# Performance work log

Measured on AMD Instinct MI355X. Metric: run time of the kernel, lower is better.

## Reference

```python
import jax, jax.numpy as jnp
import numpy as np

B, T, C, H = 2, 2048, 1024, 16
D = C // H  # head dim = 64
EPS = 1e-6  # kernel adds 1e-6 to softmax denominator


def setup_inputs() -> dict:
    key = jax.random.key(0)
    k1, k2, k3, k4, k5 = jax.random.split(key, 5)
    s = 1.0 / np.sqrt(C)
    return {
        "x": jax.random.normal(k1, (B, T, C), dtype=jnp.float32),
        "w_attn": jax.random.normal(k2, (3 * C, C), dtype=jnp.float32) * s,
        "b_attn": jax.random.normal(k3, (3 * C,), dtype=jnp.float32) * 0.02,
        "w_proj": jax.random.normal(k4, (C, C), dtype=jnp.float32) * s,
        "b_proj": jax.random.normal(k5, (C,), dtype=jnp.float32) * 0.02,
    }


def reference(x, w_attn, b_attn, w_proj, b_proj):
    b, t, c = x.shape
    qkv = x @ w_attn.T + b_attn                      # [B,T,3C]
    q, k, v = jnp.split(qkv, 3, axis=2)
    # [B,T,C] -> [B,H,T,D]
    q = q.reshape(b, t, H, D).transpose(0, 2, 1, 3)
    k = k.reshape(b, t, H, D).transpose(0, 2, 1, 3)
    v = v.reshape(b, t, H, D).transpose(0, 2, 1, 3)
    scale = 1.0 / np.sqrt(D)
    att = jnp.einsum("bhid,bhjd->bhij", q, k) * scale  # [B,H,T,T]
    causal = jnp.tril(jnp.ones((t, t), dtype=bool))
    att = jnp.where(causal, att, -jnp.inf)
    # softmax matching the HIP kernel: denom has +1e-6
    m = jnp.max(att, axis=-1, keepdims=True)
    e = jnp.exp(att - m)                             # masked entries -> 0
    p = e / (jnp.sum(e, axis=-1, keepdims=True) + EPS)
    y = jnp.einsum("bhij,bhjd->bhid", p, v)          # [B,H,T,D]
    y = y.transpose(0, 2, 1, 3).reshape(b, t, c)     # [B,T,C]
    return y @ w_proj.T + b_proj
```

## Files before the change

### kernel.cpp

```cpp
#include <hip/hip_runtime.h>

#define B_ 2
#define T_ 2048
#define C_ 1024
#define H_ 16
#define D_ 64

typedef __bf16 bf16x8 __attribute__((ext_vector_type(8)));
typedef float f32x4 __attribute__((ext_vector_type(4)));

__device__ __forceinline__ unsigned short f2bf(float f) {
  unsigned u = __float_as_uint(f);
  unsigned r = (u + 0x7fffu + ((u >> 16) & 1u)) >> 16;
  return (unsigned short)r;
}

#define NX 1048576
#define NWA 786432
#define NWP 262144
__global__ __launch_bounds__(256) void convert_all(
    const float* __restrict__ x, const float* __restrict__ wa,
    const float* __restrict__ wp, unsigned short* __restrict__ xb,
    unsigned short* __restrict__ wab, unsigned short* __restrict__ wpb) {
  int i = blockIdx.x * 256 + threadIdx.x;
  const float* s; unsigned short* d; int j;
  if (i < NX)            { s = x;  d = xb;  j = i; }
  else if (i < NX + NWA) { s = wa; d = wab; j = i - NX; }
  else                   { s = wp; d = wpb; j = i - NX - NWA; }
  float4 v = ((const float4*)s)[j];
  ushort4 u;
  u.x = f2bf(v.x); u.y = f2bf(v.y); u.z = f2bf(v.z); u.w = f2bf(v.w);
  ((ushort4*)d)[j] = u;
}

__global__ __launch_bounds__(256) void gemm_bt(
    const unsigned short* __restrict__ A,
    const unsigned short* __restrict__ Bm,
    const float* __restrict__ bias,
    int M, int N, int K, int mode,
    float* __restrict__ outf,
    unsigned short* __restrict__ qb,
    unsigned short* __restrict__ kb,
    unsigned short* __restrict__ vb) {
  __shared__ unsigned short As[128 * 64];
  __shared__ unsigned short Bs[128 * 64];

  const int tid  = threadIdx.x;
  const int lane = tid & 63;
  const int wave = tid >> 6;
  const int quad = lane >> 4;
  const int l16  = lane & 15;
  const int q4   = quad * 4;

  const int bm = blockIdx.y * 128;
  const int bn = blockIdx.x * 128;
  const int wm = (wave >> 1) * 64;
  const int wn = (wave & 1) * 64;

  f32x4 acc[4][4] = {};

  const int srow8 = lane >> 3;
  const int scol  = ((lane & 7) ^ srow8) * 8;
  const int srow  = wave * 8 + srow8;

  for (int k0 = 0; k0 < K; k0 += 64) {
#pragma unroll
    for (int c = 0; c < 4; ++c) {
      const int r = c * 32 + srow;
      const unsigned short* ga = A  + (size_t)(bm + r) * K + (k0 + scol);
      const unsigned short* gb = Bm + (size_t)(bn + r) * K + (k0 + scol);
      unsigned short* la = &As[(c * 32 + wave * 8) * 64];
      unsigned short* lb = &Bs[(c * 32 + wave * 8) * 64];
      __builtin_amdgcn_global_load_lds(
          (__attribute__((address_space(1))) unsigned int*)ga,
          (__attribute__((address_space(3))) unsigned int*)la, 16, 0, 0);
      __builtin_amdgcn_global_load_lds(
          (__attribute__((address_space(1))) unsigned int*)gb,
          (__attribute__((address_space(3))) unsigned int*)lb, 16, 0, 0);
    }
    __syncthreads();
#pragma unroll
    for (int ks = 0; ks < 2; ++ks) {
      bf16x8 af[4], bfr[4];
#pragma unroll
      for (int i = 0; i < 4; ++i)
        af[i] = *(const bf16x8*)&As[(wm + i * 16 + l16) * 64 +
                                    (((ks * 4 + quad) ^ (l16 & 7)) * 8)];
#pragma unroll
      for (int j = 0; j < 4; ++j)
        bfr[j] = *(const bf16x8*)&Bs[(wn + j * 16 + l16) * 64 +
                                     (((ks * 4 + quad) ^ (l16 & 7)) * 8)];
#pragma unroll
      for (int i = 0; i < 4; ++i)
#pragma unroll
        for (int j = 0; j < 4; ++j)
          acc[i][j] = __builtin_amdgcn_mfma_f32_16x16x32_bf16(af[i], bfr[j], acc[i][j], 0, 0, 0);
    }
    __syncthreads();
  }

#pragma unroll
  for (int j = 0; j < 4; ++j) {
    const int gn = bn + wn + j * 16 + l16;
    const float bv = bias[gn];
    if (mode == 0) {
#pragma unroll
      for (int i = 0; i < 4; ++i)
#pragma unroll
        for (int r = 0; r < 4; ++r) {
          const int gm = bm + wm + i * 16 + q4 + r;
          outf[(size_t)gm * N + gn] = acc[i][j][r] + bv;
        }
    } else {
      const int which = gn >> 10;
      const int cc = gn & 1023;
      const int h = cc >> 6, d = cc & 63;
      if (which == 2) {
#pragma unroll
        for (int i = 0; i < 4; ++i) {
          const int gm0 = bm + wm + i * 16 + q4;
          const int b = gm0 >> 11, t0 = gm0 & 2047;
          ushort4 u;
          u.x = f2bf(acc[i][j][0] + bv);
          u.y = f2bf(acc[i][j][1] + bv);
          u.z = f2bf(acc[i][j][2] + bv);
          u.w = f2bf(acc[i][j][3] + bv);
          *(ushort4*)&vb[(((size_t)(b * H_ + h) * D_) + d) * T_ + t0] = u;
        }
      } else {
        const float sc = (which == 0) ? 0.125f : 1.0f;
        unsigned short* dst = (which == 0) ? qb : kb;
#pragma unroll
        for (int i = 0; i < 4; ++i)
#pragma unroll
          for (int r = 0; r < 4; ++r) {
            const int gm = bm + wm + i * 16 + q4 + r;
            const int b = gm >> 11, t = gm & 2047;
            dst[(((size_t)(b * H_ + h) * T_) + t) * D_ + d] = f2bf((acc[i][j][r] + bv) * sc);
          }
      }
    }
  }
}

__global__ __launch_bounds__(256, 2) void attn_mfma(
    const unsigned short* __restrict__ Qb,
    const unsigned short* __restrict__ Kb,
    const unsigned short* __restrict__ Vtg,
    unsigned short* __restrict__ Yb,
    unsigned short* __restrict__ op,
    float* __restrict__ lp) {
  __shared__ unsigned short Ks[64 * 64];
  __shared__ unsigned short Vt[64 * 64];
  __shared__ unsigned short Pn[4][16 * 64];

  const int tid  = threadIdx.x;
  const int lane = tid & 63;
  const int wave = tid >> 6;
  const int quad = lane >> 4;
  const int l16  = lane & 15;
  const int q4   = quad * 4;
  const int sw   = (l16 & 7);

  const int id = blockIdx.x;
  const int bh = id / 51;
  const int w  = id - bh * 51;
  int qt = 0, nsplits = 1, pfx = 0;
  for (int q = 0; q < 16; ++q) {
    const int n = (2 * q + 7) / 6;
    if (w < pfx + n) { qt = q; nsplits = n; break; }
    pfx += n;
  }
  const int chunk = w - pfx;

  const int tiles_total = 2 * qt + 2;
  const int tpc = (tiles_total + nsplits - 1) / nsplits;
  const int t0 = chunk * tpc;
  const int t1 = min(t0 + tpc, tiles_total);

  const int b = bh >> 4, h = bh & 15;
  const size_t base = (size_t)bh * T_ * D_;
  const int wq = qt * 128 + wave * 32;
  const int wt1 = min(t1, (wq + 95) >> 6);

  bf16x8 qf[2][2];
#pragma unroll
  for (int nt = 0; nt < 2; ++nt)
#pragma unroll
    for (int ks = 0; ks < 2; ++ks)
      qf[nt][ks] = *(const bf16x8*)(Qb + base + (size_t)(wq + nt * 16 + l16) * 64 +
                                    ks * 32 + quad * 8);

  f32x4 o[4][2] = {};
  float l2[2] = {0.f, 0.f};

  const int srow8 = lane >> 3;
  const int satom = ((lane & 7) ^ srow8) * 8;

  for (int kt = t0; kt < t1; ++kt) {
    const int kt0 = kt * 64;
    __syncthreads();
#pragma unroll
    for (int c = 0; c < 2; ++c) {
      const int row = wave * 16 + c * 8 + srow8;
      const unsigned short* gk = Kb  + base + (size_t)(kt0 + row) * 64 + satom;
      const unsigned short* gv = Vtg + base + (size_t)row * T_ + kt0 + satom;
      unsigned short* lk = &Ks[(wave * 16 + c * 8) * 64];
      unsigned short* lv = &Vt[(wave * 16 + c * 8) * 64];
      __builtin_amdgcn_global_load_lds(
          (__attribute__((address_space(1))) unsigned int*)gk,
          (__attribute__((address_space(3))) unsigned int*)lk, 16, 0, 0);
      __builtin_amdgcn_global_load_lds(
          (__attribute__((address_space(1))) unsigned int*)gv,
          (__attribute__((address_space(3))) unsigned int*)lv, 16, 0, 0);
    }
    __syncthreads();

    if (kt < wt1) {
      f32x4 s[4][2] = {};
#pragma unroll
      for (int ks = 0; ks < 2; ++ks) {
        bf16x8 kf[4];
#pragma unroll
        for (int mt = 0; mt < 4; ++mt)
          kf[mt] = *(const bf16x8*)&Ks[(mt * 16 + l16) * 64 +
                                       (((ks * 4 + quad) ^ sw) * 8)];
#pragma unroll
        for (int mt = 0; mt < 4; ++mt)
#pragma unroll
          for (int nt = 0; nt < 2; ++nt)
            s[mt][nt] = __builtin_amdgcn_mfma_f32_16x16x32_bf16(kf[mt], qf[nt][ks],
                                                                s[mt][nt], 0, 0, 0);
      }
      if (kt0 + 63 > wq) {
#pragma unroll
        for (int mt = 0; mt < 4; ++mt)
#pragma unroll
          for (int nt = 0; nt < 2; ++nt)
#pragma unroll
            for (int r = 0; r < 4; ++r)
              if (kt0 + mt * 16 + q4 + r > wq + nt * 16 + l16) s[mt][nt][r] = -1e30f;
      }
#pragma unroll
      for (int nt = 0; nt < 2; ++nt) {
        float ps = 0.f;
#pragma unroll
        for (int mt = 0; mt < 4; ++mt) {
          float p0 = __expf(s[mt][nt][0]);
          float p1 = __expf(s[mt][nt][1]);
          float p2 = __expf(s[mt][nt][2]);
          float p3 = __expf(s[mt][nt][3]);
          ps += (p0 + p1) + (p2 + p3);
          unsigned lo = __builtin_amdgcn_perm(__float_as_uint(p1) + 0x8000u,
                                              __float_as_uint(p0) + 0x8000u,
                                              0x07060302u);
          unsigned hi = __builtin_amdgcn_perm(__float_as_uint(p3) + 0x8000u,
                                              __float_as_uint(p2) + 0x8000u,
                                              0x07060302u);
          uint2 pk; pk.x = lo; pk.y = hi;
          const int atom = (2 * mt + (quad >> 1)) ^ sw;
          *(uint2*)&Pn[wave][l16 * 64 + atom * 8 + (quad & 1) * 4] = pk;
        }
        l2[nt] += ps;
#pragma unroll
        for (int ks = 0; ks < 2; ++ks) {
          bf16x8 pf = *(const bf16x8*)&Pn[wave][l16 * 64 +
                                               (((ks * 4 + quad) ^ sw) * 8)];
          bf16x8 vf[4];
#pragma unroll
          for (int dt = 0; dt < 4; ++dt)
            vf[dt] = *(const bf16x8*)&Vt[(dt * 16 + l16) * 64 +
                                         (((ks * 4 + quad) ^ sw) * 8)];
#pragma unroll
          for (int dt = 0; dt < 4; ++dt)
            o[dt][nt] = __builtin_amdgcn_mfma_f32_16x16x32_bf16(vf[dt], pf,
                                                                o[dt][nt], 0, 0, 0);
        }
      }
    }
  }

#pragma unroll
  for (int nt = 0; nt < 2; ++nt) {
    float l = l2[nt];
    l += __shfl_xor(l, 16);
    l += __shfl_xor(l, 32);
    const int qloc = wave * 32 + nt * 16 + l16;
    if (nsplits == 1) {
      const float inv = 1.f / (l + 1e-6f);
      const int q = qt * 128 + qloc;
#pragma unroll
      for (int dt = 0; dt < 4; ++dt) {
        ushort4 u;
        u.x = f2bf(o[dt][nt][0] * inv);
        u.y = f2bf(o[dt][nt][1] * inv);
        u.z = f2bf(o[dt][nt][2] * inv);
        u.w = f2bf(o[dt][nt][3] * inv);
        *(ushort4*)&Yb[((size_t)(b * T_ + q)) * C_ + h * 64 + dt * 16 + q4] = u;
      }
    } else {
      if (quad == 0) lp[(size_t)id * 128 + qloc] = l;
#pragma unroll
      for (int dt = 0; dt < 4; ++dt) {
        ushort4 u;
        u.x = f2bf(o[dt][nt][0]);
        u.y = f2bf(o[dt][nt][1]);
        u.z = f2bf(o[dt][nt][2]);
        u.w = f2bf(o[dt][nt][3]);
        *(ushort4*)&op[(size_t)id * 8192 + (size_t)qloc * 64 + dt * 16 + q4] = u;
      }
    }
  }
}

__global__ __launch_bounds__(256) void attn_combine(
    const unsigned short* __restrict__ op, const float* __restrict__ lp,
    unsigned short* __restrict__ Yb) {
  const int cb = blockIdx.x;
  const int bh = cb / 13;
  const int qt = 3 + (cb - bh * 13);
  int pfx = 0;
  for (int q = 0; q < 16; ++q) {
    if (q == qt) break;
    pfx += (2 * q + 7) / 6;
  }
  const int nsplits = (2 * qt + 7) / 6;
  const int slot0 = bh * 51 + pfx;

  const int t = threadIdx.x;
  const int qloc = t >> 1;
  const int d0 = (t & 1) * 32;

  float l = 1e-6f;
  float acc[32];
#pragma unroll
  for (int i = 0; i < 32; ++i) acc[i] = 0.f;
  for (int s = 0; s < nsplits; ++s) {
    l += lp[(size_t)(slot0 + s) * 128 + qloc];
    const uint4* src = (const uint4*)(op + (size_t)(slot0 + s) * 8192 +
                                      (size_t)qloc * 64 + d0);
#pragma unroll
    for (int c = 0; c < 4; ++c) {
      uint4 v = src[c];
      acc[c*8+0] += __uint_as_float(v.x << 16);
      acc[c*8+1] += __uint_as_float(v.x & 0xffff0000u);
      acc[c*8+2] += __uint_as_float(v.y << 16);
      acc[c*8+3] += __uint_as_float(v.y & 0xffff0000u);
      acc[c*8+4] += __uint_as_float(v.z << 16);
      acc[c*8+5] += __uint_as_float(v.z & 0xffff0000u);
      acc[c*8+6] += __uint_as_float(v.w << 16);
      acc[c*8+7] += __uint_as_float(v.w & 0xffff0000u);
    }
  }
  const float inv = 1.f / l;
  const int b = bh >> 4, h = bh & 15;
  const int q = qt * 128 + qloc;
  uint4* dst = (uint4*)(Yb + ((size_t)(b * T_ + q)) * C_ + h * 64 + d0);
#pragma unroll
  for (int c = 0; c < 4; ++c) {
    uint4 v;
    v.x = (unsigned)f2bf(acc[c*8+0] * inv) | ((unsigned)f2bf(acc[c*8+1] * inv) << 16);
    v.y = (unsigned)f2bf(acc[c*8+2] * inv) | ((unsigned)f2bf(acc[c*8+3] * inv) << 16);
    v.z = (unsigned)f2bf(acc[c*8+4] * inv) | ((unsigned)f2bf(acc[c*8+5] * inv) << 16);
    v.w = (unsigned)f2bf(acc[c*8+6] * inv) | ((unsigned)f2bf(acc[c*8+7] * inv) << 16);
    dst[c] = v;
  }
}

extern "C" void kernel_launch(void* const* d_in, const int* in_sizes, int n_in,
                              void* d_out, int out_size, void* d_ws, size_t ws_size,
                              hipStream_t stream) {
  const float* x      = (const float*)d_in[0];
  const float* w_attn = (const float*)d_in[1];
  const float* b_attn = (const float*)d_in[2];
  const float* w_proj = (const float*)d_in[3];
  const float* b_proj = (const float*)d_in[4];
  float* out = (float*)d_out;

  char* ws = (char*)d_ws;
  unsigned short* xb  = (unsigned short*)ws;  ws += (size_t)4096 * 1024 * 2;
  unsigned short* wab = (unsigned short*)ws;  ws += (size_t)3072 * 1024 * 2;
  unsigned short* wpb = (unsigned short*)ws;  ws += (size_t)1024 * 1024 * 2;
  unsigned short* qb  = (unsigned short*)ws;  ws += (size_t)B_ * H_ * T_ * D_ * 2;
  unsigned short* kb  = (unsigned short*)ws;  ws += (size_t)B_ * H_ * T_ * D_ * 2;
  unsigned short* vb  = (unsigned short*)ws;  ws += (size_t)B_ * H_ * T_ * D_ * 2;
  unsigned short* yb  = (unsigned short*)ws;  ws += (size_t)4096 * 1024 * 2;
  unsigned short* op  = (unsigned short*)ws;  ws += (size_t)1632 * 128 * 64 * 2;
  float*          lp  = (float*)ws;           ws += (size_t)1632 * 128 * 4;
  (void)ws_size; (void)in_sizes; (void)n_in; (void)out_size;

  convert_all<<<8192, 256, 0, stream>>>(x, w_attn, w_proj, xb, wab, wpb);

  gemm_bt<<<dim3(24, 32), 256, 0, stream>>>(xb, wab, b_attn, 4096, 3072, 1024, 1,
                                            nullptr, qb, kb, vb);
  attn_mfma<<<1632, 256, 0, stream>>>(qb, kb, vb, yb, op, lp);
  attn_combine<<<416, 256, 0, stream>>>(op, lp, yb);
  gemm_bt<<<dim3(8, 32), 256, 0, stream>>>(yb, wpb, b_proj, 4096, 1024, 1024, 0,
                                           out, nullptr, nullptr, nullptr);
}
```

Baseline: 189.0 us.

## Load V fragments directly from global, interleave head blocks, add narrow proj GEMM

The attention kernel no longer stages V through LDS. Each wave now reads its V fragments straight from global memory, which cuts the LDS footprint and the shared-memory traffic. Block indices are remapped so consecutive blocks cover different batch-heads, with split-output slots keyed by a logical slot index to spread the causal load. The output projection moves to a new 128x64-tile GEMM launched on 512 blocks for better CU occupancy. The cost is uncached, strided global reads of V that are repeated by every wave.

Result: slower. 194.3 us (+2.8%).

```diff
diff --git a/kernel.cpp b/kernel.cpp
--- a/kernel.cpp
+++ b/kernel.cpp
@@ -143,6 +143,83 @@
   }
 }
 
+__global__ __launch_bounds__(256) void gemm_bt_n64(
+    const unsigned short* __restrict__ A,
+    const unsigned short* __restrict__ Bm,
+    const float* __restrict__ bias, int M, int N, int K,
+    float* __restrict__ outf) {
+  __shared__ unsigned short As[128 * 64];
+  __shared__ unsigned short Bs[64 * 64];
+
+  const int tid  = threadIdx.x;
+  const int lane = tid & 63;
+  const int wave = tid >> 6;
+  const int quad = lane >> 4;
+  const int l16  = lane & 15;
+  const int q4   = quad * 4;
+
+  const int bm = blockIdx.y * 128;
+  const int bn = blockIdx.x * 64;
+  const int wm = wave * 32;
+
+  f32x4 acc[2][4] = {};
+
+  const int srow8 = lane >> 3;
+  const int scol  = ((lane & 7) ^ srow8) * 8;
+  const int srow  = wave * 8 + srow8;
+
+  for (int k0 = 0; k0 < K; k0 += 64) {
+#pragma unroll
+    for (int c = 0; c < 4; ++c) {
+      const unsigned short* ga = A + (size_t)(bm + c * 32 + srow) * K + (k0 + scol);
+      __builtin_amdgcn_global_load_lds(
+          (__attribute__((address_space(1))) unsigned int*)ga,
+          (__attribute__((address_space(3))) unsigned int*)&As[(c * 32 + wave * 8) * 64],
+          16, 0, 0);
+    }
+#pragma unroll
+    for (int c = 0; c < 2; ++c) {
+      const unsigned short* gb = Bm + (size_t)(bn + c * 32 + srow) * K + (k0 + scol);
+      __builtin_amdgcn_global_load_lds(
+          (__attribute__((address_space(1))) unsigned int*)gb,
+          (__attribute__((address_space(3))) unsigned int*)&Bs[(c * 32 + wave * 8) * 64],
+          16, 0, 0);
+    }
+    __syncthreads();
+#pragma unroll
+    for (int ks = 0; ks < 2; ++ks) {
+      bf16x8 af[2], bfr[4];
+#pragma unroll
+      for (int i = 0; i < 2; ++i)
+        af[i] = *(const bf16x8*)&As[(wm + i * 16 + l16) * 64 +
+                                    (((ks * 4 + quad) ^ (l16 & 7)) * 8)];
+#pragma unroll
+      for (int j = 0; j < 4; ++j)
+        bfr[j] = *(const bf16x8*)&Bs[(j * 16 + l16) * 64 +
+                                     (((ks * 4 + quad) ^ (l16 & 7)) * 8)];
+#pragma unroll
+      for (int i = 0; i < 2; ++i)
+#pragma unroll
+        for (int j = 0; j < 4; ++j)
+          acc[i][j] = __builtin_amdgcn_mfma_f32_16x16x32_bf16(af[i], bfr[j], acc[i][j], 0, 0, 0);
+    }
+    __syncthreads();
+  }
+
+#pragma unroll
+  for (int j = 0; j < 4; ++j) {
+    const int gn = bn + j * 16 + l16;
+    const float bv = bias[gn];
+#pragma unroll
+    for (int i = 0; i < 2; ++i)
+#pragma unroll
+      for (int r = 0; r < 4; ++r) {
+        const int gm = bm + wm + i * 16 + q4 + r;
+        outf[(size_t)gm * N + gn] = acc[i][j][r] + bv;
+      }
+  }
+}
+
 __global__ __launch_bounds__(256, 2) void attn_mfma(
     const unsigned short* __restrict__ Qb,
     const unsigned short* __restrict__ Kb,
@@ -151,7 +228,6 @@
     unsigned short* __restrict__ op,
     float* __restrict__ lp) {
   __shared__ unsigned short Ks[64 * 64];
-  __shared__ unsigned short Vt[64 * 64];
   __shared__ unsigned short Pn[4][16 * 64];
 
   const int tid  = threadIdx.x;
@@ -163,8 +239,8 @@
   const int sw   = (l16 & 7);
 
   const int id = blockIdx.x;
-  const int bh = id / 51;
-  const int w  = id - bh * 51;
+  const int bh = id & 31;
+  const int w  = id >> 5;
   int qt = 0, nsplits = 1, pfx = 0;
   for (int q = 0; q < 16; ++q) {
     const int n = (2 * q + 7) / 6;
@@ -172,6 +248,7 @@
     pfx += n;
   }
   const int chunk = w - pfx;
+  const int slot = bh * 51 + w;
 
   const int tiles_total = 2 * qt + 2;
   const int tpc = (tiles_total + nsplits - 1) / nsplits;
@@ -196,6 +273,7 @@
 
   const int srow8 = lane >> 3;
   const int satom = ((lane & 7) ^ srow8) * 8;
+  const unsigned short* vbase = Vtg + base;
 
   for (int kt = t0; kt < t1; ++kt) {
     const int kt0 = kt * 64;
@@ -203,20 +281,22 @@
 #pragma unroll
     for (int c = 0; c < 2; ++c) {
       const int row = wave * 16 + c * 8 + srow8;
-      const unsigned short* gk = Kb  + base + (size_t)(kt0 + row) * 64 + satom;
-      const unsigned short* gv = Vtg + base + (size_t)row * T_ + kt0 + satom;
-      unsigned short* lk = &Ks[(wave * 16 + c * 8) * 64];
-      unsigned short* lv = &Vt[(wave * 16 + c * 8) * 64];
+      const unsigned short* gk = Kb + base + (size_t)(kt0 + row) * 64 + satom;
       __builtin_amdgcn_global_load_lds(
           (__attribute__((address_space(1))) unsigned int*)gk,
-          (__attribute__((address_space(3))) unsigned int*)lk, 16, 0, 0);
-      __builtin_amdgcn_global_load_lds(
-          (__attribute__((address_space(1))) unsigned int*)gv,
-          (__attribute__((address_space(3))) unsigned int*)lv, 16, 0, 0);
+          (__attribute__((address_space(3))) unsigned int*)&Ks[(wave * 16 + c * 8) * 64],
+          16, 0, 0);
     }
     __syncthreads();
 
     if (kt < wt1) {
+      bf16x8 vf[4][2];
+#pragma unroll
+      for (int dt = 0; dt < 4; ++dt)
+#pragma unroll
+        for (int ks = 0; ks < 2; ++ks)
+          vf[dt][ks] = *(const bf16x8*)(vbase + (size_t)(dt * 16 + l16) * T_ +
+                                        kt0 + ks * 32 + quad * 8);
       f32x4 s[4][2] = {};
 #pragma unroll
       for (int ks = 0; ks < 2; ++ks) {
@@ -266,14 +346,9 @@
         for (int ks = 0; ks < 2; ++ks) {
           bf16x8 pf = *(const bf16x8*)&Pn[wave][l16 * 64 +
                                                (((ks * 4 + quad) ^ sw) * 8)];
-          bf16x8 vf[4];
 #pragma unroll
           for (int dt = 0; dt < 4; ++dt)
-            vf[dt] = *(const bf16x8*)&Vt[(dt * 16 + l16) * 64 +
-                                         (((ks * 4 + quad) ^ sw) * 8)];
-#pragma unroll
-          for (int dt = 0; dt < 4; ++dt)
-            o[dt][nt] = __builtin_amdgcn_mfma_f32_16x16x32_bf16(vf[dt], pf,
+            o[dt][nt] = __builtin_amdgcn_mfma_f32_16x16x32_bf16(vf[dt][ks], pf,
                                                                 o[dt][nt], 0, 0, 0);
         }
       }
@@ -299,7 +374,7 @@
         *(ushort4*)&Yb[((size_t)(b * T_ + q)) * C_ + h * 64 + dt * 16 + q4] = u;
       }
     } else {
-      if (quad == 0) lp[(size_t)id * 128 + qloc] = l;
+      if (quad == 0) lp[(size_t)slot * 128 + qloc] = l;
 #pragma unroll
       for (int dt = 0; dt < 4; ++dt) {
         ushort4 u;
@@ -307,7 +382,7 @@
         u.y = f2bf(o[dt][nt][1]);
         u.z = f2bf(o[dt][nt][2]);
         u.w = f2bf(o[dt][nt][3]);
-        *(ushort4*)&op[(size_t)id * 8192 + (size_t)qloc * 64 + dt * 16 + q4] = u;
+        *(ushort4*)&op[(size_t)slot * 8192 + (size_t)qloc * 64 + dt * 16 + q4] = u;
       }
     }
   }
@@ -395,6 +470,5 @@
                                             nullptr, qb, kb, vb);
   attn_mfma<<<1632, 256, 0, stream>>>(qb, kb, vb, yb, op, lp);
   attn_combine<<<416, 256, 0, stream>>>(op, lp, yb);
-  gemm_bt<<<dim3(8, 32), 256, 0, stream>>>(yb, wpb, b_proj, 4096, 1024, 1024, 0,
-                                           out, nullptr, nullptr, nullptr);
-}
+  gemm_bt_n64<<<dim3(16, 32), 256, 0, stream>>>(yb, wpb, b_proj, 4096, 1024, 1024, out);
+}
```
